# Kernel tuning notes

Hardware: AMD Instinct MI355X
Metric: run time of the kernel (lower is better)

Reference implementation:

```python
import jax, jax.numpy as jnp
import numpy as np

N = 100000   # nodes
E = 1600000  # edges
D = 64       # in_dim == hidden
H = 64       # hidden
L = 5        # GIN layers
G = 128      # graphs in batch
OUT = 10     # out_dim
BN_EPS = 1e-5


def setup_inputs() -> dict:
    key = jax.random.key(0)
    ks = jax.random.split(key, 16)
    x = jax.random.normal(ks[0], (N, D), dtype=jnp.float32)
    ei = jax.random.randint(ks[1], (2, E), 0, N, dtype=jnp.int64)
    b = jnp.sort(jax.random.randint(ks[2], (N,), 0, G, dtype=jnp.int64))
    s = 0.1
    return {
        "x": x,
        "ei": ei,
        "b": b,
        "conv_W1": jax.random.normal(ks[3], (L, D, H), dtype=jnp.float32) * s,
        "conv_b1": jnp.zeros((L, H), dtype=jnp.float32),
        "conv_W2": jax.random.normal(ks[4], (L, H, H), dtype=jnp.float32) * s,
        "conv_b2": jnp.zeros((L, H), dtype=jnp.float32),
        "bn_gamma": jnp.ones((L, H), dtype=jnp.float32),
        "bn_beta": jnp.zeros((L, H), dtype=jnp.float32),
        "head_W1": jax.random.normal(ks[5], (H, H), dtype=jnp.float32) * s,
        "head_b1": jnp.zeros((H,), dtype=jnp.float32),
        "head_W2": jax.random.normal(ks[6], (H, OUT), dtype=jnp.float32) * s,
        "head_b2": jnp.zeros((OUT,), dtype=jnp.float32),
    }


def reference(x, ei, b, conv_W1, conv_b1, conv_W2, conv_b2,
              bn_gamma, bn_beta, head_W1, head_b1, head_W2, head_b2):
    src, dst = ei[0], ei[1]
    for l in range(L):
        # GINConv (eps=0): h = x + sum_{j in N(i)} x_j  via gather + scatter-add
        agg = jax.ops.segment_sum(x[src], dst, num_segments=N)  # [N, d]
        h = x + agg
        # nn MLP: Linear -> ReLU -> Linear
        h = jax.nn.relu(h @ conv_W1[l] + conv_b1[l]) @ conv_W2[l] + conv_b2[l]
        # BatchNorm over node dim (batch statistics), then ReLU (dropout: eval)
        mean = jnp.mean(h, axis=0)
        var = jnp.var(h, axis=0)
        h = bn_gamma[l] * (h - mean) * jax.lax.rsqrt(var + BN_EPS) + bn_beta[l]
        x = jax.nn.relu(h)
    # global mean pool per graph
    sums = jax.ops.segment_sum(x, b, num_segments=G)                 # [G, H]
    cnts = jax.ops.segment_sum(jnp.ones((N,), x.dtype), b, num_segments=G)
    pooled = sums / jnp.maximum(cnts, 1.0)[:, None]
    # head: Linear -> ReLU -> (Dropout eval) -> Linear
    return jax.nn.relu(pooled @ head_W1 + head_b1) @ head_W2 + head_b2
```

## Files before the change

### kernel.cpp

```cpp
#include <hip/hip_runtime.h>

#define N_NODES 100000
#define N_EDGES 1600000
#define HDIM    64
#define NLAYERS 5
#define NGRAPH  128
#define NOUT    10
#define BN_EPS  1e-5f


__global__ __launch_bounds__(256) void k_hist(const int* __restrict__ dst, int* __restrict__ counts) {
    int e = blockIdx.x * 256 + threadIdx.x;
    if (e < N_EDGES) atomicAdd(&counts[dst[e]], 1);
}

__global__ __launch_bounds__(256) void k_scan_bt(const int* __restrict__ counts, int* __restrict__ bsums) {
    __shared__ int sm[256];
    int t = threadIdx.x;
    int base = blockIdx.x * 1024 + t * 4;
    int s = 0;
#pragma unroll
    for (int k = 0; k < 4; ++k) { int i = base + k; s += (i < N_NODES) ? counts[i] : 0; }
    sm[t] = s; __syncthreads();
    for (int o = 128; o > 0; o >>= 1) { if (t < o) sm[t] += sm[t + o]; __syncthreads(); }
    if (t == 0) bsums[blockIdx.x] = sm[0];
}

__global__ void k_scan_tot(int* bsums, int nblk, int* offsets) {
    if (threadIdx.x == 0 && blockIdx.x == 0) {
        int run = 0;
        for (int i = 0; i < nblk; ++i) { int v = bsums[i]; bsums[i] = run; run += v; }
        offsets[N_NODES] = N_EDGES;
    }
}

__global__ __launch_bounds__(256) void k_scan_fin(const int* __restrict__ counts, const int* __restrict__ bsums,
                                                 int* __restrict__ offsets, int* __restrict__ cursor) {
    __shared__ int sm[256];
    int t = threadIdx.x;
    int base = blockIdx.x * 1024 + t * 4;
    int v[4]; int s = 0;
#pragma unroll
    for (int k = 0; k < 4; ++k) { int i = base + k; v[k] = (i < N_NODES) ? counts[i] : 0; s += v[k]; }
    sm[t] = s; __syncthreads();
    for (int o = 1; o < 256; o <<= 1) {
        int add = (t >= o) ? sm[t - o] : 0;
        __syncthreads();
        sm[t] += add;
        __syncthreads();
    }
    int run = bsums[blockIdx.x] + (sm[t] - s);
#pragma unroll
    for (int k = 0; k < 4; ++k) {
        int i = base + k;
        if (i < N_NODES) { offsets[i] = run; cursor[i] = run; run += v[k]; }
    }
}

__global__ __launch_bounds__(256) void k_fill(const int* __restrict__ src, const int* __restrict__ dst,
                                              int* __restrict__ cursor, int* __restrict__ csr) {
    int e = blockIdx.x * 256 + threadIdx.x;
    if (e < N_EDGES) {
        int d = dst[e];
        int p = atomicAdd(&cursor[d], 1);
        csr[p] = src[e];
    }
}


static __device__ __forceinline__ void bn_coeffs(const float* stats, const float* gam, const float* bet,
                                                 int j0, float4& sc, float4& sh) {
    const float invN = 1.0f / (float)N_NODES;
    float m, v, s;
    m = stats[j0+0]*invN; v = stats[64+j0+0]*invN - m*m; s = gam[j0+0]*rsqrtf(v+BN_EPS); sc.x = s; sh.x = bet[j0+0]-m*s;
    m = stats[j0+1]*invN; v = stats[64+j0+1]*invN - m*m; s = gam[j0+1]*rsqrtf(v+BN_EPS); sc.y = s; sh.y = bet[j0+1]-m*s;
    m = stats[j0+2]*invN; v = stats[64+j0+2]*invN - m*m; s = gam[j0+2]*rsqrtf(v+BN_EPS); sc.z = s; sh.z = bet[j0+2]-m*s;
    m = stats[j0+3]*invN; v = stats[64+j0+3]*invN - m*m; s = gam[j0+3]*rsqrtf(v+BN_EPS); sc.w = s; sh.w = bet[j0+3]-m*s;
}

static __device__ __forceinline__ float4 bn_apply(float4 v, const float4& sc, const float4& sh) {
    v.x = fmaxf(fmaf(v.x, sc.x, sh.x), 0.f);
    v.y = fmaxf(fmaf(v.y, sc.y, sh.y), 0.f);
    v.z = fmaxf(fmaf(v.z, sc.z, sh.z), 0.f);
    v.w = fmaxf(fmaf(v.w, sc.w, sh.w), 0.f);
    return v;
}

template <bool APPLY>
__global__ __launch_bounds__(256) void k_agg(const float4* __restrict__ x4, const int* __restrict__ offsets,
                                             const int* __restrict__ csr, float4* __restrict__ agg4,
                                             const float* __restrict__ stats, const float* __restrict__ gam,
                                             const float* __restrict__ bet) {
    int tid = blockIdx.x * 256 + threadIdx.x;
    int n = tid >> 4, q = tid & 15;
    if (n >= N_NODES) return;
    float4 sc, sh;
    if (APPLY) bn_coeffs(stats, gam, bet, q * 4, sc, sh);
    int beg = offsets[n], end = offsets[n + 1];
    float4 a0 = make_float4(0.f, 0.f, 0.f, 0.f);
    float4 a1 = make_float4(0.f, 0.f, 0.f, 0.f);
    int e = beg;
    for (; e + 1 < end; e += 2) {
        int s0 = csr[e], s1 = csr[e + 1];
        float4 v0 = x4[(size_t)s0 * 16 + q];
        float4 v1 = x4[(size_t)s1 * 16 + q];
        if (APPLY) { v0 = bn_apply(v0, sc, sh); v1 = bn_apply(v1, sc, sh); }
        a0.x += v0.x; a0.y += v0.y; a0.z += v0.z; a0.w += v0.w;
        a1.x += v1.x; a1.y += v1.y; a1.z += v1.z; a1.w += v1.w;
    }
    if (e < end) {
        int s0 = csr[e];
        float4 v0 = x4[(size_t)s0 * 16 + q];
        if (APPLY) v0 = bn_apply(v0, sc, sh);
        a0.x += v0.x; a0.y += v0.y; a0.z += v0.z; a0.w += v0.w;
    }
    a0.x += a1.x; a0.y += a1.y; a0.z += a1.z; a0.w += a1.w;
    agg4[(size_t)n * 16 + q] = a0;
}

#define MLP_TB 128
#define ROWS   68
template <bool APPLY>
__global__ __launch_bounds__(MLP_TB) void k_mlp2(const float* __restrict__ x, float* __restrict__ aggh2,
                                                 const float* __restrict__ W1, const float* __restrict__ b1,
                                                 const float* __restrict__ W2, const float* __restrict__ b2,
                                                 const float* __restrict__ statsPrev, const float* __restrict__ gam,
                                                 const float* __restrict__ bet, float* __restrict__ statsOut) {
    __shared__ float sm[MLP_TB * ROWS];
    __shared__ float red1[MLP_TB], red2[MLP_TB];
    int t = threadIdx.x;
    int base = blockIdx.x * MLP_TB;
    {
        int q = t & 15;
        float4 sc, sh;
        if (APPLY) bn_coeffs(statsPrev, gam, bet, q * 4, sc, sh);
        for (int i = t; i < MLP_TB * 16; i += MLP_TB) {
            int r = i >> 4;
            int n = base + r; if (n >= N_NODES) n = N_NODES - 1;
            float4 xv = ((const float4*)x)[(size_t)n * 16 + q];
            if (APPLY) xv = bn_apply(xv, sc, sh);
            float4 av = ((const float4*)aggh2)[(size_t)n * 16 + q];
            float4 s; s.x = xv.x + av.x; s.y = xv.y + av.y; s.z = xv.z + av.z; s.w = xv.w + av.w;
            *((float4*)&sm[r * ROWS + q * 4]) = s;
        }
    }
    __syncthreads();
    int n = base + t;
    bool valid = n < N_NODES;
    float* row = &sm[t * ROWS];
    float acc[64];
#pragma unroll
    for (int j = 0; j < 64; ++j) acc[j] = b1[j];
    for (int k = 0; k < 64; ++k) {
        float xk = row[k];
        const float* w = &W1[k * 64];
#pragma unroll
        for (int j = 0; j < 64; ++j) acc[j] = fmaf(xk, w[j], acc[j]);
    }
#pragma unroll
    for (int q = 0; q < 16; ++q) {
        float4 h;
        h.x = fmaxf(acc[4 * q + 0], 0.f);
        h.y = fmaxf(acc[4 * q + 1], 0.f);
        h.z = fmaxf(acc[4 * q + 2], 0.f);
        h.w = fmaxf(acc[4 * q + 3], 0.f);
        *((float4*)&row[q * 4]) = h;
    }
#pragma unroll
    for (int j = 0; j < 64; ++j) acc[j] = b2[j];
    for (int k = 0; k < 64; ++k) {
        float xk = row[k];
        const float* w = &W2[k * 64];
#pragma unroll
        for (int j = 0; j < 64; ++j) acc[j] = fmaf(xk, w[j], acc[j]);
    }
    if (valid) {
        float4* o = (float4*)(aggh2 + (size_t)n * 64);
#pragma unroll
        for (int q = 0; q < 16; ++q)
            o[q] = make_float4(acc[4 * q + 0], acc[4 * q + 1], acc[4 * q + 2], acc[4 * q + 3]);
    }
#pragma unroll
    for (int q = 0; q < 16; ++q) {
        float4 h;
        if (valid) h = make_float4(acc[4*q+0], acc[4*q+1], acc[4*q+2], acc[4*q+3]);
        else       h = make_float4(0.f, 0.f, 0.f, 0.f);
        *((float4*)&row[q * 4]) = h;
    }
    __syncthreads();
    {
        int j = t & 63, half = t >> 6;
        float s = 0.f, sq = 0.f;
        const float* col = &sm[(half * 64) * ROWS + j];
#pragma unroll 8
        for (int r = 0; r < 64; ++r) { float v = col[r * ROWS]; s += v; sq += v * v; }
        red1[t] = s; red2[t] = sq;
    }
    __syncthreads();
    if (t < 64) {
        atomicAdd(&statsOut[t], red1[t] + red1[t + 64]);
    } else {
        int j = t - 64;
        atomicAdd(&statsOut[64 + j], red2[j] + red2[j + 64]);
    }
}


__global__ void k_bounds(const int* __restrict__ b, int* __restrict__ bounds) {
    int g = threadIdx.x;
    if (g > NGRAPH) return;
    int lo = 0, hi = N_NODES;
    while (lo < hi) { int mid = (lo + hi) >> 1; if (b[mid] < g) lo = mid + 1; else hi = mid; }
    bounds[g] = lo;
}

__global__ __launch_bounds__(256) void k_pool(const float4* __restrict__ x4, const int* __restrict__ bounds,
                                              float4* __restrict__ pooled4, const float* __restrict__ stats,
                                              const float* __restrict__ gam, const float* __restrict__ bet) {
    int g = blockIdx.x;
    int beg = bounds[g], end = bounds[g + 1];
    int t = threadIdx.x;
    int q = t & 15;
    int w = t >> 4;
    float4 sc, sh;
    bn_coeffs(stats, gam, bet, q * 4, sc, sh);
    float4 a = make_float4(0.f, 0.f, 0.f, 0.f);
    for (int n = beg + w; n < end; n += 16) {
        float4 v = bn_apply(x4[(size_t)n * 16 + q], sc, sh);
        a.x += v.x; a.y += v.y; a.z += v.z; a.w += v.w;
    }
    __shared__ float4 sm[16][16];
    sm[w][q] = a; __syncthreads();
    for (int o = 8; o > 0; o >>= 1) {
        if (w < o) {
            float4 u = sm[w + o][q];
            sm[w][q].x += u.x; sm[w][q].y += u.y; sm[w][q].z += u.z; sm[w][q].w += u.w;
        }
        __syncthreads();
    }
    if (w == 0) {
        float inv = (end > beg) ? 1.0f / (float)(end - beg) : 0.0f;
        float4 r = sm[0][q];
        r.x *= inv; r.y *= inv; r.z *= inv; r.w *= inv;
        pooled4[g * 16 + q] = r;
    }
}

__global__ __launch_bounds__(128) void k_head(const float* __restrict__ pooled,
                                              const float* __restrict__ W1, const float* __restrict__ b1,
                                              const float* __restrict__ W2, const float* __restrict__ b2,
                                              float* __restrict__ out) {
    __shared__ float w1s[64 * 64];
    __shared__ float w2s[64 * NOUT];
    int t = threadIdx.x;
    for (int i = t; i < 64 * 64; i += 128) w1s[i] = W1[i];
    for (int i = t; i < 64 * NOUT; i += 128) w2s[i] = W2[i];
    __syncthreads();
    int g = t;
    float pr[64];
#pragma unroll
    for (int k = 0; k < 64; ++k) pr[k] = pooled[g * 64 + k];
    float acc[NOUT];
#pragma unroll
    for (int o = 0; o < NOUT; ++o) acc[o] = b2[o];
    for (int j = 0; j < 64; ++j) {
        float h = b1[j];
#pragma unroll
        for (int k = 0; k < 64; ++k) h = fmaf(pr[k], w1s[k * 64 + j], h);
        h = fmaxf(h, 0.f);
#pragma unroll
        for (int o = 0; o < NOUT; ++o) acc[o] = fmaf(h, w2s[j * NOUT + o], acc[o]);
    }
#pragma unroll
    for (int o = 0; o < NOUT; ++o) out[g * NOUT + o] = acc[o];
}


extern "C" void kernel_launch(void* const* d_in, const int* in_sizes, int n_in,
                              void* d_out, int out_size, void* d_ws, size_t ws_size,
                              hipStream_t stream) {
    const float* x0  = (const float*)d_in[0];
    const int*   ei  = (const int*)d_in[1];
    const int*   b   = (const int*)d_in[2];
    const float* cW1 = (const float*)d_in[3];
    const float* cb1 = (const float*)d_in[4];
    const float* cW2 = (const float*)d_in[5];
    const float* cb2 = (const float*)d_in[6];
    const float* gam = (const float*)d_in[7];
    const float* bet = (const float*)d_in[8];
    const float* hW1 = (const float*)d_in[9];
    const float* hb1 = (const float*)d_in[10];
    const float* hW2 = (const float*)d_in[11];
    const float* hb2 = (const float*)d_in[12];
    float* out = (float*)d_out;

    char* ws = (char*)d_ws;
    size_t off = 0;
    auto alloc = [&](size_t bytes) { void* p = ws + off; off += (bytes + 255) & ~(size_t)255; return p; };
    float* bufA   = (float*)alloc((size_t)N_NODES * 64 * sizeof(float));
    float* bufB   = (float*)alloc((size_t)N_NODES * 64 * sizeof(float));
    int*   csr    = (int*)alloc((size_t)N_EDGES * sizeof(int));
    int*   counts = (int*)alloc((size_t)(N_NODES + 1) * sizeof(int));
    int*   offs   = (int*)alloc((size_t)(N_NODES + 1) * sizeof(int));
    int*   cursor = (int*)alloc((size_t)(N_NODES + 1) * sizeof(int));
    int*   bsums  = (int*)alloc(256 * sizeof(int));
    float* stats  = (float*)alloc(NLAYERS * 128 * sizeof(float));
    float* pooled = (float*)alloc(NGRAPH * 64 * sizeof(float));
    int*   bounds = (int*)alloc((NGRAPH + 1) * sizeof(int));

    const int* src = ei;
    const int* dst = ei + N_EDGES;

    hipMemsetAsync(counts, 0, (N_NODES + 1) * sizeof(int), stream);
    hipMemsetAsync(stats, 0, NLAYERS * 128 * sizeof(float), stream);

    const int EB = (N_EDGES + 255) / 256;
    const int SB = (N_NODES + 1023) / 1024;
    k_hist<<<EB, 256, 0, stream>>>(dst, counts);
    k_scan_bt<<<SB, 256, 0, stream>>>(counts, bsums);
    k_scan_tot<<<1, 1, 0, stream>>>(bsums, SB, offs);
    k_scan_fin<<<SB, 256, 0, stream>>>(counts, bsums, offs, cursor);
    k_fill<<<EB, 256, 0, stream>>>(src, dst, cursor, csr);
    k_bounds<<<1, NGRAPH + 1, 0, stream>>>(b, bounds);

    const int AB = (N_NODES * 16 + 255) / 256;
    const int MB_G = (N_NODES + MLP_TB - 1) / MLP_TB;

    const float* P = x0;
    float* Q = bufA;
    float* spare = bufB;
    for (int l = 0; l < NLAYERS; ++l) {
        const float* sPrev = stats + (size_t)(l - 1) * 128;
        const float* gPrev = gam + (size_t)(l - 1) * 64;
        const float* bPrev = bet + (size_t)(l - 1) * 64;
        if (l == 0) {
            k_agg<false><<<AB, 256, 0, stream>>>((const float4*)P, offs, csr, (float4*)Q,
                                                 nullptr, nullptr, nullptr);
            k_mlp2<false><<<MB_G, MLP_TB, 0, stream>>>(P, Q,
                                                       cW1, cb1, cW2, cb2,
                                                       nullptr, nullptr, nullptr, stats);
        } else {
            k_agg<true><<<AB, 256, 0, stream>>>((const float4*)P, offs, csr, (float4*)Q,
                                                sPrev, gPrev, bPrev);
            k_mlp2<true><<<MB_G, MLP_TB, 0, stream>>>(P, Q,
                                                      cW1 + (size_t)l * 64 * 64, cb1 + l * 64,
                                                      cW2 + (size_t)l * 64 * 64, cb2 + l * 64,
                                                      sPrev, gPrev, bPrev, stats + (size_t)l * 128);
        }
        float* newSpare = (P == x0) ? spare : (float*)P;
        P = Q;
        Q = newSpare;
        spare = nullptr;
    }

    k_pool<<<NGRAPH, 256, 0, stream>>>((const float4*)P, bounds, (float4*)pooled,
                                       stats + 4 * 128, gam + 4 * 64, bet + 4 * 64);
    k_head<<<1, 128, 0, stream>>>(pooled, hW1, hb1, hW2, hb2, out);
}
```

Measured before the change: 893.0 us.

## Build CSR via two-pass bucketed binning instead of random-scatter atomic fill

Replaces the single-pass CSR fill, which did one global atomic and one random write per edge, with two passes. First, edges are binned into 196 buckets of 512 destination nodes each, using shared-memory counting and a block-local sort, with (local dst, src) packed into one 32-bit word. Second, each bucket's edges are scattered into the CSR, so cursor atomics and writes stay within a small region. This adds two kernels and an extra pass over a temporary buffer that reuses bufB, in exchange for better locality. The packing assumes node ids fit in 17 bits.

```diff
diff --git a/kernel.cpp b/kernel.cpp
--- a/kernel.cpp
+++ b/kernel.cpp
@@ -7,6 +7,8 @@
 #define NGRAPH  128
 #define NOUT    10
 #define BN_EPS  1e-5f
+#define NBUCK   196
+#define EPB     8192
 
 
 __global__ __launch_bounds__(256) void k_hist(const int* __restrict__ dst, int* __restrict__ counts) {
@@ -57,13 +59,77 @@
     }
 }
 
-__global__ __launch_bounds__(256) void k_fill(const int* __restrict__ src, const int* __restrict__ dst,
-                                              int* __restrict__ cursor, int* __restrict__ csr) {
-    int e = blockIdx.x * 256 + threadIdx.x;
-    if (e < N_EDGES) {
-        int d = dst[e];
-        int p = atomicAdd(&cursor[d], 1);
-        csr[p] = src[e];
+__global__ void k_binit(const int* __restrict__ offs, int* __restrict__ bcursor) {
+    int b = blockIdx.x * 256 + threadIdx.x;
+    if (b < NBUCK) bcursor[b] = offs[b << 9];
+}
+
+__global__ __launch_bounds__(1024) void k_binfill(const int* __restrict__ src, const int* __restrict__ dst,
+                                                  int* __restrict__ bcursor, unsigned* __restrict__ tmp) {
+    __shared__ unsigned slots[EPB];
+    __shared__ int cnt[NBUCK], lcur[NBUCK], gbase[NBUCK];
+    __shared__ int lbase[NBUCK + 1];
+    __shared__ int sscan[256];
+    int t = threadIdx.x;
+    int e0 = blockIdx.x * EPB;
+    for (int i = t; i < NBUCK; i += 1024) { cnt[i] = 0; lcur[i] = 0; }
+    __syncthreads();
+    unsigned pk[8]; int bk[8];
+#pragma unroll
+    for (int k = 0; k < 8; ++k) {
+        int e = e0 + k * 1024 + t;
+        bk[k] = -1;
+        if (e < N_EDGES) {
+            int s = src[e], d = dst[e];
+            int b = d >> 9;
+            pk[k] = ((unsigned)(d & 511) << 17) | (unsigned)s;
+            bk[k] = b;
+            atomicAdd(&cnt[b], 1);
+        }
+    }
+    __syncthreads();
+    if (t < 256) sscan[t] = (t < NBUCK) ? cnt[t] : 0;
+    __syncthreads();
+    for (int o = 1; o < 256; o <<= 1) {
+        int v = 0;
+        if (t < 256 && t >= o) v = sscan[t - o];
+        __syncthreads();
+        if (t < 256) sscan[t] += v;
+        __syncthreads();
+    }
+    if (t < NBUCK) {
+        lbase[t] = sscan[t] - cnt[t];
+        gbase[t] = atomicAdd(&bcursor[t], cnt[t]);
+    }
+    if (t == 0) lbase[NBUCK] = sscan[255];
+    __syncthreads();
+#pragma unroll
+    for (int k = 0; k < 8; ++k) {
+        if (bk[k] >= 0) {
+            int pos = lbase[bk[k]] + atomicAdd(&lcur[bk[k]], 1);
+            slots[pos] = pk[k];
+        }
+    }
+    __syncthreads();
+    int total = lbase[NBUCK];
+    for (int i = t; i < total; i += 1024) {
+        int lo = 0, hi = NBUCK - 1;
+        while (lo < hi) { int mid = (lo + hi + 1) >> 1; if (lbase[mid] <= i) lo = mid; else hi = mid - 1; }
+        tmp[gbase[lo] + (i - lbase[lo])] = slots[i];
+    }
+}
+
+__global__ __launch_bounds__(1024) void k_localcsr(const unsigned* __restrict__ tmp, const int* __restrict__ offs,
+                                                   int* __restrict__ cursor, int* __restrict__ csr) {
+    int b = blockIdx.x;
+    int nlo = b << 9;
+    int nhi = nlo + 512; if (nhi > N_NODES) nhi = N_NODES;
+    int base = offs[nlo], end = offs[nhi];
+    for (int i = base + (int)threadIdx.x; i < end; i += 1024) {
+        unsigned pk = tmp[i];
+        int node = nlo + (int)(pk >> 17);
+        int p = atomicAdd(&cursor[node], 1);
+        csr[p] = (int)(pk & 0x1FFFFu);
     }
 }
 
@@ -304,9 +370,11 @@
     int*   offs   = (int*)alloc((size_t)(N_NODES + 1) * sizeof(int));
     int*   cursor = (int*)alloc((size_t)(N_NODES + 1) * sizeof(int));
     int*   bsums  = (int*)alloc(256 * sizeof(int));
+    int*   bcursor= (int*)alloc(256 * sizeof(int));
     float* stats  = (float*)alloc(NLAYERS * 128 * sizeof(float));
     float* pooled = (float*)alloc(NGRAPH * 64 * sizeof(float));
     int*   bounds = (int*)alloc((NGRAPH + 1) * sizeof(int));
+    unsigned* tmp = (unsigned*)bufB;
 
     const int* src = ei;
     const int* dst = ei + N_EDGES;
@@ -316,11 +384,14 @@
 
     const int EB = (N_EDGES + 255) / 256;
     const int SB = (N_NODES + 1023) / 1024;
+    const int FB = (N_EDGES + EPB - 1) / EPB;
     k_hist<<<EB, 256, 0, stream>>>(dst, counts);
     k_scan_bt<<<SB, 256, 0, stream>>>(counts, bsums);
     k_scan_tot<<<1, 1, 0, stream>>>(bsums, SB, offs);
     k_scan_fin<<<SB, 256, 0, stream>>>(counts, bsums, offs, cursor);
-    k_fill<<<EB, 256, 0, stream>>>(src, dst, cursor, csr);
+    k_binit<<<1, 256, 0, stream>>>(offs, bcursor);
+    k_binfill<<<FB, 1024, 0, stream>>>(src, dst, bcursor, tmp);
+    k_localcsr<<<NBUCK, 1024, 0, stream>>>(tmp, offs, cursor, csr);
     k_bounds<<<1, NGRAPH + 1, 0, stream>>>(b, bounds);
 
     const int AB = (N_NODES * 16 + 255) / 256;
@@ -350,7 +421,6 @@
         float* newSpare = (P == x0) ? spare : (float*)P;
         P = Q;
         Q = newSpare;
-        spare = nullptr;
     }
 
     k_pool<<<NGRAPH, 256, 0, stream>>>((const float4*)P, bounds, (float4*)pooled,
```

New measurement: 830.2 us. 1.08x faster.
